# Optimization experiments

Measured on AMD Instinct MI355X. Metric: run time of the kernel, lower is better.

The kernel has to match this reference:

```python
import jax, jax.numpy as jnp
import numpy as np

N = 2048
DT = 0.016
GRAVITY = jnp.array([0.0, -9.8, 0.0], dtype=jnp.float32)


def setup_inputs() -> dict:
    key = jax.random.key(0)
    ks = jax.random.split(key, 10)

    def init_w(k, shape):
        # torch Linear default: U(-1/sqrt(fan_in), 1/sqrt(fan_in)); approximate scale
        bound = 1.0 / np.sqrt(shape[0])
        return jax.random.uniform(k, shape, jnp.float32, -bound, bound)

    return {
        "external_forces": jax.random.normal(ks[0], (N, 3), jnp.float32),
        "positions": jax.random.normal(ks[1], (N, 3), jnp.float32) * 0.1,
        "velocities": jnp.zeros((N, 3), jnp.float32),
        "mass": jnp.ones((N,), jnp.float32),
        "elasticity": jnp.full((N,), 0.8, jnp.float32),
        "friction": jnp.full((N,), 0.1, jnp.float32),
        "W1": init_w(ks[2], (8, 64)),  "b1": jnp.zeros((64,), jnp.float32),
        "W2": init_w(ks[3], (64, 64)), "b2": jnp.zeros((64,), jnp.float32),
        "W3": init_w(ks[4], (64, 32)), "b3": jnp.zeros((32,), jnp.float32),
        "W4": init_w(ks[5], (32, 3)),  "b4": jnp.zeros((3,), jnp.float32),
    }


def _force_mlp(f, W1, b1, W2, b2, W3, b3, W4, b4):
    h = jax.nn.relu(f @ W1 + b1)
    h = jax.nn.relu(h @ W2 + b2)
    h = jax.nn.relu(h @ W3 + b3)
    return jnp.tanh(h @ W4 + b4) * 10.0


def _neural_forces(positions, velocities, mass, W1, b1, W2, b2, W3, b3, W4, b4):
    # edge (i, j): features = [pos_j - pos_i, vel_j - vel_i, dist_ij, mass_i / mass_j]
    rel_pos = positions[None, :, :] - positions[:, None, :]          # [N, N, 3]
    rel_vel = velocities[None, :, :] - velocities[:, None, :]        # [N, N, 3]
    dist = jnp.linalg.norm(rel_pos, axis=-1)                          # [N, N]
    ratio = mass[:, None] / mass[None, :]                             # [N, N]
    feat = jnp.concatenate(
        [rel_pos, rel_vel, dist[..., None], ratio[..., None]], axis=-1)  # [N, N, 8]
    edge_f = _force_mlp(feat, W1, b1, W2, b2, W3, b3, W4, b4)         # [N, N, 3]
    mask = (dist < 1.0) & ~jnp.eye(dist.shape[0], dtype=bool)         # radius graph, no self-edge
    return jnp.sum(edge_f * mask[..., None], axis=1)                  # scatter-add over j -> [N, 3]


def reference(external_forces, positions, velocities, mass, elasticity, friction,
              W1, b1, W2, b2, W3, b3, W4, b4):
    forces = GRAVITY[None, :] * mass[:, None] + external_forces
    forces = forces + _neural_forces(positions, velocities, mass,
                                     W1, b1, W2, b2, W3, b3, W4, b4)
    accel = forces / mass[:, None]
    new_vel = velocities + accel * DT
    # friction applied where |v| > 0.1
    fric_mask = jnp.linalg.norm(new_vel, axis=1) > 0.1
    new_vel = new_vel + jnp.where(fric_mask[:, None],
                                  -new_vel * friction[:, None] * DT, 0.0)
    new_pos = positions + new_vel * DT
    # ground collision: clamp y, reflect vy scaled by elasticity
    coll = new_pos[:, 1] < 0.0
    new_pos = new_pos.at[:, 1].set(jnp.where(coll, 0.0, new_pos[:, 1]))
    new_vel = new_vel.at[:, 1].set(
        jnp.where(coll, -new_vel[:, 1] * elasticity, new_vel[:, 1]))
    return new_pos, new_vel
```

## Files before the change

kernel.cpp:

```cpp
#include <hip/hip_runtime.h>
#include <math.h>

#define NPART 2048
#define DT 0.016f

typedef __attribute__((ext_vector_type(8)))  short bf16x8;
typedef __attribute__((ext_vector_type(16))) float f32x16;

#define MFMA(A, B, C) __builtin_amdgcn_mfma_f32_32x32x16_bf16((A), (B), (C), 0, 0, 0)

__device__ inline unsigned cvt_pk(float lo, float hi) {
    unsigned r;
    asm("v_cvt_pk_bf16_f32 %0, %1, %2" : "=v"(r) : "v"(lo), "v"(hi));
    return r;
}
__device__ inline void swap32(unsigned &x, unsigned &y) {
    asm("v_permlane32_swap_b32 %0, %1" : "+v"(x), "+v"(y));
}
__device__ inline bf16x8 mk8(unsigned a, unsigned b, unsigned c, unsigned d) {
    union { unsigned u[4]; bf16x8 s; } u;
    u.u[0] = a; u.u[1] = b; u.u[2] = c; u.u[3] = d;
    return u.s;
}
__device__ inline bf16x8 pack8(const float f[8]) {
    return mk8(cvt_pk(f[0], f[1]), cvt_pk(f[2], f[3]), cvt_pk(f[4], f[5]), cvt_pk(f[6], f[7]));
}

__device__ inline void d2b(const f32x16 &d, bf16x8 &blo, bf16x8 &bhi) {
    float r[16];
#pragma unroll
    for (int t = 0; t < 16; ++t) r[t] = fmaxf(d[t], 0.f);
    unsigned p01 = cvt_pk(r[0], r[1]),  p23 = cvt_pk(r[2], r[3]);
    unsigned p45 = cvt_pk(r[4], r[5]),  p67 = cvt_pk(r[6], r[7]);
    swap32(p01, p45);
    swap32(p23, p67);
    blo = mk8(p01, p23, p45, p67);
    unsigned q01 = cvt_pk(r[8], r[9]),   q23 = cvt_pk(r[10], r[11]);
    unsigned q45 = cvt_pk(r[12], r[13]), q67 = cvt_pk(r[14], r[15]);
    swap32(q01, q45);
    swap32(q23, q67);
    bhi = mk8(q01, q23, q45, q67);
}

__global__ __launch_bounds__(256) void particle_step_kernel(
    const float* __restrict__ ext,  const float* __restrict__ pos,
    const float* __restrict__ vel,  const float* __restrict__ mass,
    const float* __restrict__ elast, const float* __restrict__ fric,
    const float* __restrict__ W1, const float* __restrict__ b1,
    const float* __restrict__ W2, const float* __restrict__ b2,
    const float* __restrict__ W3, const float* __restrict__ b3,
    const float* __restrict__ W4, const float* __restrict__ b4,
    float* __restrict__ out)
{
    const int l = threadIdx.x & 63;
    const int c = l & 31;
    const int h = l >> 5;
    const int w = threadIdx.x >> 6;
    const int i = blockIdx.x;

    bf16x8 a1[2];
    bf16x8 a2[2][5];
    bf16x8 a3[5];
    bf16x8 a4[3];
#pragma unroll
    for (int mt = 0; mt < 2; ++mt) {
        const int m = c + 32 * mt;
        float f[8];
        if (h == 0) {
#pragma unroll
            for (int e = 0; e < 8; ++e) f[e] = W1[e * 64 + m];
        } else {
            f[0] = b1[m];
#pragma unroll
            for (int e = 1; e < 8; ++e) f[e] = 0.f;
        }
        a1[mt] = pack8(f);
    }
#pragma unroll
    for (int mt = 0; mt < 2; ++mt) {
        const int m = c + 32 * mt;
#pragma unroll
        for (int kg = 0; kg < 4; ++kg) {
            float f[8];
#pragma unroll
            for (int e = 0; e < 8; ++e) f[e] = W2[(kg * 16 + 8 * h + e) * 64 + m];
            a2[mt][kg] = pack8(f);
        }
        float f[8];
        f[0] = (h == 0) ? b2[m] : 0.f;
#pragma unroll
        for (int e = 1; e < 8; ++e) f[e] = 0.f;
        a2[mt][4] = pack8(f);
    }
#pragma unroll
    for (int kg = 0; kg < 4; ++kg) {
        float f[8];
#pragma unroll
        for (int e = 0; e < 8; ++e) f[e] = W3[(kg * 16 + 8 * h + e) * 32 + c];
        a3[kg] = pack8(f);
    }
    {
        float f[8];
        f[0] = (h == 0) ? b3[c] : 0.f;
#pragma unroll
        for (int e = 1; e < 8; ++e) f[e] = 0.f;
        a3[4] = pack8(f);
    }
#pragma unroll
    for (int kg = 0; kg < 2; ++kg) {
        float f[8];
#pragma unroll
        for (int e = 0; e < 8; ++e) f[e] = (c < 3) ? W4[(kg * 16 + 8 * h + e) * 3 + c] : 0.f;
        a4[kg] = pack8(f);
    }
    {
        float f[8];
        f[0] = (h == 0 && c < 3) ? b4[c] : 0.f;
#pragma unroll
        for (int e = 1; e < 8; ++e) f[e] = 0.f;
        a4[2] = pack8(f);
    }

    const bf16x8 bgate = mk8((l < 32) ? 0x00003f80u : 0u, 0u, 0u, 0u);
    const f32x16 z = {};

    const float pix = pos[3 * i], piy = pos[3 * i + 1], piz = pos[3 * i + 2];
    const float vix = vel[3 * i], viy = vel[3 * i + 1], viz = vel[3 * i + 2];
    const float mi = mass[i];

    float Fx = 0.f, Fy = 0.f, Fz = 0.f;

    for (int t = 0; t < 16; ++t) {
        const int T = w * 16 + t;
        const int j = T * 32 + c;

        const float pjx = pos[3 * j], pjy = pos[3 * j + 1], pjz = pos[3 * j + 2];
        const float vjx = vel[3 * j], vjy = vel[3 * j + 1], vjz = vel[3 * j + 2];
        const float mj = mass[j];
        const float rx = pjx - pix, ry = pjy - piy, rz = pjz - piz;
        const float sx = vjx - vix, sy = vjy - viy, sz = vjz - viz;
        const float dist = sqrtf(rx * rx + ry * ry + rz * rz);
        const float ratio = mi / mj;
        const bool valid = (dist < 1.0f) && (j != i);

        bf16x8 bf;
        if (l < 32)
            bf = mk8(cvt_pk(rx, ry), cvt_pk(rz, sx), cvt_pk(sy, sz), cvt_pk(dist, ratio));
        else
            bf = mk8(0x00003f80u, 0u, 0u, 0u);

        f32x16 acc0 = MFMA(a1[0], bf, z);
        f32x16 acc1 = MFMA(a1[1], bf, z);

        bf16x8 bn[4];
        d2b(acc0, bn[0], bn[1]);
        d2b(acc1, bn[2], bn[3]);

        acc0 = MFMA(a2[0][0], bn[0], z);
        acc0 = MFMA(a2[0][1], bn[1], acc0);
        acc0 = MFMA(a2[0][2], bn[2], acc0);
        acc0 = MFMA(a2[0][3], bn[3], acc0);
        acc0 = MFMA(a2[0][4], bgate, acc0);
        acc1 = MFMA(a2[1][0], bn[0], z);
        acc1 = MFMA(a2[1][1], bn[1], acc1);
        acc1 = MFMA(a2[1][2], bn[2], acc1);
        acc1 = MFMA(a2[1][3], bn[3], acc1);
        acc1 = MFMA(a2[1][4], bgate, acc1);

        d2b(acc0, bn[0], bn[1]);
        d2b(acc1, bn[2], bn[3]);

        f32x16 acc3 = MFMA(a3[0], bn[0], z);
        acc3 = MFMA(a3[1], bn[1], acc3);
        acc3 = MFMA(a3[2], bn[2], acc3);
        acc3 = MFMA(a3[3], bn[3], acc3);
        acc3 = MFMA(a3[4], bgate, acc3);

        bf16x8 b4lo, b4hi;
        d2b(acc3, b4lo, b4hi);

        f32x16 o = MFMA(a4[0], b4lo, z);
        o = MFMA(a4[1], b4hi, o);
        o = MFMA(a4[2], bgate, o);

        if (l < 32 && valid) {
            Fx += tanhf(o[0]) * 10.f;
            Fy += tanhf(o[1]) * 10.f;
            Fz += tanhf(o[2]) * 10.f;
        }
    }

#pragma unroll
    for (int off = 1; off < 64; off <<= 1) {
        Fx += __shfl_xor(Fx, off);
        Fy += __shfl_xor(Fy, off);
        Fz += __shfl_xor(Fz, off);
    }
    __shared__ float red[4][3];
    if ((threadIdx.x & 63) == 0) { red[w][0] = Fx; red[w][1] = Fy; red[w][2] = Fz; }
    __syncthreads();

    if (threadIdx.x == 0) {
        float FX = red[0][0] + red[1][0] + red[2][0] + red[3][0];
        float FY = red[0][1] + red[1][1] + red[2][1] + red[3][1];
        float FZ = red[0][2] + red[1][2] + red[2][2] + red[3][2];

        FX += ext[3 * i + 0];
        FY += ext[3 * i + 1] + (-9.8f) * mi;
        FZ += ext[3 * i + 2];

        const float inv_m = 1.0f / mi;
        float nvx = vix + FX * inv_m * DT;
        float nvy = viy + FY * inv_m * DT;
        float nvz = viz + FZ * inv_m * DT;

        const float speed = sqrtf(nvx * nvx + nvy * nvy + nvz * nvz);
        if (speed > 0.1f) {
            const float s = fric[i] * DT;
            nvx -= nvx * s;
            nvy -= nvy * s;
            nvz -= nvz * s;
        }

        float npx = pix + nvx * DT;
        float npy = piy + nvy * DT;
        float npz = piz + nvz * DT;

        if (npy < 0.0f) {
            npy = 0.0f;
            nvy = -nvy * elast[i];
        }

        out[3 * i + 0] = npx;
        out[3 * i + 1] = npy;
        out[3 * i + 2] = npz;
        out[NPART * 3 + 3 * i + 0] = nvx;
        out[NPART * 3 + 3 * i + 1] = nvy;
        out[NPART * 3 + 3 * i + 2] = nvz;
    }
}

extern "C" void kernel_launch(void* const* d_in, const int* in_sizes, int n_in,
                              void* d_out, int out_size, void* d_ws, size_t ws_size,
                              hipStream_t stream) {
    const float* ext   = (const float*)d_in[0];
    const float* pos   = (const float*)d_in[1];
    const float* vel   = (const float*)d_in[2];
    const float* mass  = (const float*)d_in[3];
    const float* elast = (const float*)d_in[4];
    const float* fric  = (const float*)d_in[5];
    const float* W1 = (const float*)d_in[6];
    const float* b1 = (const float*)d_in[7];
    const float* W2 = (const float*)d_in[8];
    const float* b2 = (const float*)d_in[9];
    const float* W3 = (const float*)d_in[10];
    const float* b3 = (const float*)d_in[11];
    const float* W4 = (const float*)d_in[12];
    const float* b4 = (const float*)d_in[13];
    float* out = (float*)d_out;

    particle_step_kernel<<<NPART, 256, 0, stream>>>(
        ext, pos, vel, mass, elast, fric,
        W1, b1, W2, b2, W3, b3, W4, b4, out);
}
```

Baseline: 115.8 us.

## Switch MLP to fp16 MFMA and add split-precision fixup pass for boundary particles

Replaces the bf16 MFMAs with fp16 MFMAs and uses a fast exp/rcp tanh, a branchless masked accumulate, and interleaved layer-2 accumulator chains. The main kernel records the pre-clamp y position in workspace. A second kernel recomputes particles whose y lies within a small margin of zero using hi/lo split fp16 (roughly 3x MFMA work), so the ground-collision branch decision matches the fp32 reference. This adds a second launch and heavier recompute for near-boundary particles in exchange for a cheaper, more accurate main path.

```diff
diff --git a/kernel.cpp b/kernel.cpp
--- a/kernel.cpp
+++ b/kernel.cpp
@@ -3,43 +3,78 @@
 
 #define NPART 2048
 #define DT 0.016f
-
-typedef __attribute__((ext_vector_type(8)))  short bf16x8;
+#define MARGIN_EPS 2e-3f
+
+typedef _Float16 f16x8 __attribute__((ext_vector_type(8)));
 typedef __attribute__((ext_vector_type(16))) float f32x16;
 
-#define MFMA(A, B, C) __builtin_amdgcn_mfma_f32_32x32x16_bf16((A), (B), (C), 0, 0, 0)
-
-__device__ inline unsigned cvt_pk(float lo, float hi) {
-    unsigned r;
-    asm("v_cvt_pk_bf16_f32 %0, %1, %2" : "=v"(r) : "v"(lo), "v"(hi));
-    return r;
+#define MFMA(A, B, C) __builtin_amdgcn_mfma_f32_32x32x16_f16((A), (B), (C), 0, 0, 0)
+
+__device__ inline unsigned pk16(float lo, float hi) {
+    union { _Float16 h[2]; unsigned u; } x;
+    x.h[0] = (_Float16)lo; x.h[1] = (_Float16)hi;
+    return x.u;
 }
 __device__ inline void swap32(unsigned &x, unsigned &y) {
     asm("v_permlane32_swap_b32 %0, %1" : "+v"(x), "+v"(y));
 }
-__device__ inline bf16x8 mk8(unsigned a, unsigned b, unsigned c, unsigned d) {
-    union { unsigned u[4]; bf16x8 s; } u;
+__device__ inline f16x8 mk8(unsigned a, unsigned b, unsigned c, unsigned d) {
+    union { unsigned u[4]; f16x8 s; } u;
     u.u[0] = a; u.u[1] = b; u.u[2] = c; u.u[3] = d;
     return u.s;
 }
-__device__ inline bf16x8 pack8(const float f[8]) {
-    return mk8(cvt_pk(f[0], f[1]), cvt_pk(f[2], f[3]), cvt_pk(f[4], f[5]), cvt_pk(f[6], f[7]));
-}
-
-__device__ inline void d2b(const f32x16 &d, bf16x8 &blo, bf16x8 &bhi) {
+__device__ inline f16x8 pack8(const float f[8]) {
+    return mk8(pk16(f[0], f[1]), pk16(f[2], f[3]), pk16(f[4], f[5]), pk16(f[6], f[7]));
+}
+
+__device__ inline float tanh10(float x) {
+    float e;
+    asm("v_exp_f32 %0, %1" : "=v"(e) : "v"(x * 2.885390081777927f));
+    float r;
+    asm("v_rcp_f32 %0, %1" : "=v"(r) : "v"(e + 1.0f));
+    return fmaf(-20.f, r, 10.f);
+}
+
+__device__ inline void d2b(const f32x16 &d, f16x8 &blo, f16x8 &bhi) {
     float r[16];
 #pragma unroll
     for (int t = 0; t < 16; ++t) r[t] = fmaxf(d[t], 0.f);
-    unsigned p01 = cvt_pk(r[0], r[1]),  p23 = cvt_pk(r[2], r[3]);
-    unsigned p45 = cvt_pk(r[4], r[5]),  p67 = cvt_pk(r[6], r[7]);
+    unsigned p01 = pk16(r[0], r[1]),  p23 = pk16(r[2], r[3]);
+    unsigned p45 = pk16(r[4], r[5]),  p67 = pk16(r[6], r[7]);
     swap32(p01, p45);
     swap32(p23, p67);
     blo = mk8(p01, p23, p45, p67);
-    unsigned q01 = cvt_pk(r[8], r[9]),   q23 = cvt_pk(r[10], r[11]);
-    unsigned q45 = cvt_pk(r[12], r[13]), q67 = cvt_pk(r[14], r[15]);
+    unsigned q01 = pk16(r[8], r[9]),   q23 = pk16(r[10], r[11]);
+    unsigned q45 = pk16(r[12], r[13]), q67 = pk16(r[14], r[15]);
     swap32(q01, q45);
     swap32(q23, q67);
     bhi = mk8(q01, q23, q45, q67);
+}
+
+__device__ inline void d2b_split(const f32x16 &d, f16x8 &h0, f16x8 &h1, f16x8 &l0, f16x8 &l1) {
+    float r[16];
+#pragma unroll
+    for (int t = 0; t < 16; ++t) r[t] = fmaxf(d[t], 0.f);
+    unsigned ph[8], pl[8];
+#pragma unroll
+    for (int q = 0; q < 8; ++q) {
+        const float a = r[2 * q], b = r[2 * q + 1];
+        const _Float16 ha = (_Float16)a, hb = (_Float16)b;
+        union { _Float16 h[2]; unsigned u; } up;
+        up.h[0] = ha; up.h[1] = hb;
+        ph[q] = up.u;
+        union { _Float16 h[2]; unsigned u; } ul;
+        ul.h[0] = (_Float16)(a - (float)ha); ul.h[1] = (_Float16)(b - (float)hb);
+        pl[q] = ul.u;
+    }
+    swap32(ph[0], ph[2]); swap32(ph[1], ph[3]);
+    h0 = mk8(ph[0], ph[1], ph[2], ph[3]);
+    swap32(ph[4], ph[6]); swap32(ph[5], ph[7]);
+    h1 = mk8(ph[4], ph[5], ph[6], ph[7]);
+    swap32(pl[0], pl[2]); swap32(pl[1], pl[3]);
+    l0 = mk8(pl[0], pl[1], pl[2], pl[3]);
+    swap32(pl[4], pl[6]); swap32(pl[5], pl[7]);
+    l1 = mk8(pl[4], pl[5], pl[6], pl[7]);
 }
 
 __global__ __launch_bounds__(256) void particle_step_kernel(
@@ -50,7 +85,7 @@
     const float* __restrict__ W2, const float* __restrict__ b2,
     const float* __restrict__ W3, const float* __restrict__ b3,
     const float* __restrict__ W4, const float* __restrict__ b4,
-    float* __restrict__ out)
+    float* __restrict__ out, float* __restrict__ ws)
 {
     const int l = threadIdx.x & 63;
     const int c = l & 31;
@@ -58,10 +93,7 @@
     const int w = threadIdx.x >> 6;
     const int i = blockIdx.x;
 
-    bf16x8 a1[2];
-    bf16x8 a2[2][5];
-    bf16x8 a3[5];
-    bf16x8 a4[3];
+    f16x8 a1[2], a2[2][5], a3[5], a4[3];
 #pragma unroll
     for (int mt = 0; mt < 2; ++mt) {
         const int m = c + 32 * mt;
@@ -121,7 +153,7 @@
         a4[2] = pack8(f);
     }
 
-    const bf16x8 bgate = mk8((l < 32) ? 0x00003f80u : 0u, 0u, 0u, 0u);
+    const f16x8 bgate = mk8((l < 32) ? 0x00003C00u : 0u, 0u, 0u, 0u);
     const f32x16 z = {};
 
     const float pix = pos[3 * i], piy = pos[3 * i + 1], piz = pos[3 * i + 2];
@@ -131,40 +163,41 @@
     float Fx = 0.f, Fy = 0.f, Fz = 0.f;
 
     for (int t = 0; t < 16; ++t) {
-        const int T = w * 16 + t;
-        const int j = T * 32 + c;
+        const int j = (w * 16 + t) * 32 + c;
 
         const float pjx = pos[3 * j], pjy = pos[3 * j + 1], pjz = pos[3 * j + 2];
         const float vjx = vel[3 * j], vjy = vel[3 * j + 1], vjz = vel[3 * j + 2];
         const float mj = mass[j];
         const float rx = pjx - pix, ry = pjy - piy, rz = pjz - piz;
         const float sx = vjx - vix, sy = vjy - viy, sz = vjz - viz;
-        const float dist = sqrtf(rx * rx + ry * ry + rz * rz);
-        const float ratio = mi / mj;
-        const bool valid = (dist < 1.0f) && (j != i);
-
-        bf16x8 bf;
-        if (l < 32)
-            bf = mk8(cvt_pk(rx, ry), cvt_pk(rz, sx), cvt_pk(sy, sz), cvt_pk(dist, ratio));
-        else
-            bf = mk8(0x00003f80u, 0u, 0u, 0u);
+        const float d2 = rx * rx + ry * ry + rz * rz;
+        const float dist = __builtin_amdgcn_sqrtf(d2);
+        const float ratio = mi * __builtin_amdgcn_rcpf(mj);
+        const float sel = (l < 32 && dist < 1.0f && j != i) ? 1.0f : 0.0f;
+
+        const unsigned d0 = pk16(rx, ry), d1 = pk16(rz, sx);
+        const unsigned d2p = pk16(sy, sz), d3 = pk16(dist, ratio);
+        const f16x8 bf = mk8((l < 32) ? d0 : 0x00003C00u,
+                             (l < 32) ? d1 : 0u,
+                             (l < 32) ? d2p : 0u,
+                             (l < 32) ? d3 : 0u);
 
         f32x16 acc0 = MFMA(a1[0], bf, z);
         f32x16 acc1 = MFMA(a1[1], bf, z);
 
-        bf16x8 bn[4];
+        f16x8 bn[4];
         d2b(acc0, bn[0], bn[1]);
         d2b(acc1, bn[2], bn[3]);
 
         acc0 = MFMA(a2[0][0], bn[0], z);
+        acc1 = MFMA(a2[1][0], bn[0], z);
         acc0 = MFMA(a2[0][1], bn[1], acc0);
+        acc1 = MFMA(a2[1][1], bn[1], acc1);
         acc0 = MFMA(a2[0][2], bn[2], acc0);
+        acc1 = MFMA(a2[1][2], bn[2], acc1);
         acc0 = MFMA(a2[0][3], bn[3], acc0);
+        acc1 = MFMA(a2[1][3], bn[3], acc1);
         acc0 = MFMA(a2[0][4], bgate, acc0);
-        acc1 = MFMA(a2[1][0], bn[0], z);
-        acc1 = MFMA(a2[1][1], bn[1], acc1);
-        acc1 = MFMA(a2[1][2], bn[2], acc1);
-        acc1 = MFMA(a2[1][3], bn[3], acc1);
         acc1 = MFMA(a2[1][4], bgate, acc1);
 
         d2b(acc0, bn[0], bn[1]);
@@ -176,18 +209,244 @@
         acc3 = MFMA(a3[3], bn[3], acc3);
         acc3 = MFMA(a3[4], bgate, acc3);
 
-        bf16x8 b4lo, b4hi;
+        f16x8 b4lo, b4hi;
         d2b(acc3, b4lo, b4hi);
 
         f32x16 o = MFMA(a4[0], b4lo, z);
         o = MFMA(a4[1], b4hi, o);
         o = MFMA(a4[2], bgate, o);
 
-        if (l < 32 && valid) {
-            Fx += tanhf(o[0]) * 10.f;
-            Fy += tanhf(o[1]) * 10.f;
-            Fz += tanhf(o[2]) * 10.f;
-        }
+        Fx = fmaf(sel, tanh10(o[0]), Fx);
+        Fy = fmaf(sel, tanh10(o[1]), Fy);
+        Fz = fmaf(sel, tanh10(o[2]), Fz);
+    }
+
+#pragma unroll
+    for (int off = 1; off < 64; off <<= 1) {
+        Fx += __shfl_xor(Fx, off);
+        Fy += __shfl_xor(Fy, off);
+        Fz += __shfl_xor(Fz, off);
+    }
+    __shared__ float red[4][3];
+    if ((threadIdx.x & 63) == 0) { red[w][0] = Fx; red[w][1] = Fy; red[w][2] = Fz; }
+    __syncthreads();
+
+    if (threadIdx.x == 0) {
+        float FX = red[0][0] + red[1][0] + red[2][0] + red[3][0];
+        float FY = red[0][1] + red[1][1] + red[2][1] + red[3][1];
+        float FZ = red[0][2] + red[1][2] + red[2][2] + red[3][2];
+
+        FX += ext[3 * i + 0];
+        FY += ext[3 * i + 1] + (-9.8f) * mi;
+        FZ += ext[3 * i + 2];
+
+        const float inv_m = 1.0f / mi;
+        float nvx = vix + FX * inv_m * DT;
+        float nvy = viy + FY * inv_m * DT;
+        float nvz = viz + FZ * inv_m * DT;
+
+        const float speed = sqrtf(nvx * nvx + nvy * nvy + nvz * nvz);
+        if (speed > 0.1f) {
+            const float s = fric[i] * DT;
+            nvx -= nvx * s;
+            nvy -= nvy * s;
+            nvz -= nvz * s;
+        }
+
+        float npx = pix + nvx * DT;
+        float npy = piy + nvy * DT;
+        float npz = piz + nvz * DT;
+
+        ws[i] = npy;
+
+        if (npy < 0.0f) {
+            npy = 0.0f;
+            nvy = -nvy * elast[i];
+        }
+
+        out[3 * i + 0] = npx;
+        out[3 * i + 1] = npy;
+        out[3 * i + 2] = npz;
+        out[NPART * 3 + 3 * i + 0] = nvx;
+        out[NPART * 3 + 3 * i + 1] = nvy;
+        out[NPART * 3 + 3 * i + 2] = nvz;
+    }
+}
+
+__global__ __launch_bounds__(256, 1) void particle_fix_kernel(
+    const float* __restrict__ ext,  const float* __restrict__ pos,
+    const float* __restrict__ vel,  const float* __restrict__ mass,
+    const float* __restrict__ elast, const float* __restrict__ fric,
+    const float* __restrict__ W1, const float* __restrict__ b1,
+    const float* __restrict__ W2, const float* __restrict__ b2,
+    const float* __restrict__ W3, const float* __restrict__ b3,
+    const float* __restrict__ W4, const float* __restrict__ b4,
+    float* __restrict__ out, const float* __restrict__ ws)
+{
+    const int i = blockIdx.x;
+    if (fabsf(ws[i]) >= MARGIN_EPS) return;
+
+    const int l = threadIdx.x & 63;
+    const int c = l & 31;
+    const int h = l >> 5;
+    const int w = threadIdx.x >> 6;
+
+    f16x8 a1h[2], a1l[2];
+    f16x8 a2h[2][4], a2l[2][4];
+    f16x8 a3h[4], a3l[4];
+    f16x8 a4h[2], a4l[2];
+#pragma unroll
+    for (int mt = 0; mt < 2; ++mt) {
+        const int m = c + 32 * mt;
+        float fh[8], fl[8];
+#pragma unroll
+        for (int e = 0; e < 8; ++e) {
+            const float v = W1[e * 64 + m];
+            const float vh = (float)(_Float16)v;
+            fh[e] = vh; fl[e] = v - vh;
+        }
+        a1h[mt] = pack8(fh); a1l[mt] = pack8(fl);
+    }
+#pragma unroll
+    for (int mt = 0; mt < 2; ++mt) {
+        const int m = c + 32 * mt;
+#pragma unroll
+        for (int kg = 0; kg < 4; ++kg) {
+            float fh[8], fl[8];
+#pragma unroll
+            for (int e = 0; e < 8; ++e) {
+                const float v = W2[(kg * 16 + 8 * h + e) * 64 + m];
+                const float vh = (float)(_Float16)v;
+                fh[e] = vh; fl[e] = v - vh;
+            }
+            a2h[mt][kg] = pack8(fh); a2l[mt][kg] = pack8(fl);
+        }
+    }
+#pragma unroll
+    for (int kg = 0; kg < 4; ++kg) {
+        float fh[8], fl[8];
+#pragma unroll
+        for (int e = 0; e < 8; ++e) {
+            const float v = W3[(kg * 16 + 8 * h + e) * 32 + c];
+            const float vh = (float)(_Float16)v;
+            fh[e] = vh; fl[e] = v - vh;
+        }
+        a3h[kg] = pack8(fh); a3l[kg] = pack8(fl);
+    }
+#pragma unroll
+    for (int kg = 0; kg < 2; ++kg) {
+        float fh[8], fl[8];
+#pragma unroll
+        for (int e = 0; e < 8; ++e) {
+            const float v = (c < 3) ? W4[(kg * 16 + 8 * h + e) * 3 + c] : 0.f;
+            const float vh = (float)(_Float16)v;
+            fh[e] = vh; fl[e] = v - vh;
+        }
+        a4h[kg] = pack8(fh); a4l[kg] = pack8(fl);
+    }
+
+    f32x16 cb1a, cb1b, cb2a, cb2b, cb3, cb4;
+#pragma unroll
+    for (int t = 0; t < 16; ++t) {
+        const int row = (t & 3) + 8 * (t >> 2) + 4 * h;
+        cb1a[t] = b1[row];       cb1b[t] = b1[32 + row];
+        cb2a[t] = b2[row];       cb2b[t] = b2[32 + row];
+        cb3[t]  = b3[row];
+        cb4[t]  = (row < 3) ? b4[row] : 0.f;
+    }
+
+    const float pix = pos[3 * i], piy = pos[3 * i + 1], piz = pos[3 * i + 2];
+    const float vix = vel[3 * i], viy = vel[3 * i + 1], viz = vel[3 * i + 2];
+    const float mi = mass[i];
+
+    float Fx = 0.f, Fy = 0.f, Fz = 0.f;
+
+    for (int t = 0; t < 16; ++t) {
+        const int j = (w * 16 + t) * 32 + c;
+
+        const float pjx = pos[3 * j], pjy = pos[3 * j + 1], pjz = pos[3 * j + 2];
+        const float vjx = vel[3 * j], vjy = vel[3 * j + 1], vjz = vel[3 * j + 2];
+        const float mj = mass[j];
+        const float rx = pjx - pix, ry = pjy - piy, rz = pjz - piz;
+        const float sx = vjx - vix, sy = vjy - viy, sz = vjz - viz;
+        const float d2 = rx * rx + ry * ry + rz * rz;
+        const float dist = sqrtf(d2);
+        const float ratio = mi / mj;
+        const float sel = (l < 32 && dist < 1.0f && j != i) ? 1.0f : 0.0f;
+
+        float f8[8] = { rx, ry, rz, sx, sy, sz, dist, ratio };
+        float fh[8], fl[8];
+#pragma unroll
+        for (int e = 0; e < 8; ++e) {
+            const float vh = (float)(_Float16)f8[e];
+            fh[e] = vh; fl[e] = f8[e] - vh;
+        }
+        const f16x8 bfh = pack8(fh), bfl = pack8(fl);
+        const f16x8 bf = (l < 32) ? bfh : bfl;
+
+        f32x16 acc0 = MFMA(a1h[0], bf, cb1a);
+        acc0 = MFMA(a1l[0], bf, acc0);
+        f32x16 acc1 = MFMA(a1h[1], bf, cb1b);
+        acc1 = MFMA(a1l[1], bf, acc1);
+
+        f16x8 bh0, bh1, bh2, bh3, bl0, bl1, bl2, bl3;
+        d2b_split(acc0, bh0, bh1, bl0, bl1);
+        d2b_split(acc1, bh2, bh3, bl2, bl3);
+
+        acc0 = MFMA(a2h[0][0], bh0, cb2a);
+        acc0 = MFMA(a2h[0][1], bh1, acc0);
+        acc0 = MFMA(a2h[0][2], bh2, acc0);
+        acc0 = MFMA(a2h[0][3], bh3, acc0);
+        acc0 = MFMA(a2h[0][0], bl0, acc0);
+        acc0 = MFMA(a2h[0][1], bl1, acc0);
+        acc0 = MFMA(a2h[0][2], bl2, acc0);
+        acc0 = MFMA(a2h[0][3], bl3, acc0);
+        acc0 = MFMA(a2l[0][0], bh0, acc0);
+        acc0 = MFMA(a2l[0][1], bh1, acc0);
+        acc0 = MFMA(a2l[0][2], bh2, acc0);
+        acc0 = MFMA(a2l[0][3], bh3, acc0);
+        acc1 = MFMA(a2h[1][0], bh0, cb2b);
+        acc1 = MFMA(a2h[1][1], bh1, acc1);
+        acc1 = MFMA(a2h[1][2], bh2, acc1);
+        acc1 = MFMA(a2h[1][3], bh3, acc1);
+        acc1 = MFMA(a2h[1][0], bl0, acc1);
+        acc1 = MFMA(a2h[1][1], bl1, acc1);
+        acc1 = MFMA(a2h[1][2], bl2, acc1);
+        acc1 = MFMA(a2h[1][3], bl3, acc1);
+        acc1 = MFMA(a2l[1][0], bh0, acc1);
+        acc1 = MFMA(a2l[1][1], bh1, acc1);
+        acc1 = MFMA(a2l[1][2], bh2, acc1);
+        acc1 = MFMA(a2l[1][3], bh3, acc1);
+
+        d2b_split(acc0, bh0, bh1, bl0, bl1);
+        d2b_split(acc1, bh2, bh3, bl2, bl3);
+
+        f32x16 acc3 = MFMA(a3h[0], bh0, cb3);
+        acc3 = MFMA(a3h[1], bh1, acc3);
+        acc3 = MFMA(a3h[2], bh2, acc3);
+        acc3 = MFMA(a3h[3], bh3, acc3);
+        acc3 = MFMA(a3h[0], bl0, acc3);
+        acc3 = MFMA(a3h[1], bl1, acc3);
+        acc3 = MFMA(a3h[2], bl2, acc3);
+        acc3 = MFMA(a3h[3], bl3, acc3);
+        acc3 = MFMA(a3l[0], bh0, acc3);
+        acc3 = MFMA(a3l[1], bh1, acc3);
+        acc3 = MFMA(a3l[2], bh2, acc3);
+        acc3 = MFMA(a3l[3], bh3, acc3);
+
+        f16x8 th0, th1, tl0, tl1;
+        d2b_split(acc3, th0, th1, tl0, tl1);
+
+        f32x16 o = MFMA(a4h[0], th0, cb4);
+        o = MFMA(a4h[1], th1, o);
+        o = MFMA(a4h[0], tl0, o);
+        o = MFMA(a4h[1], tl1, o);
+        o = MFMA(a4l[0], th0, o);
+        o = MFMA(a4l[1], th1, o);
+
+        Fx = fmaf(sel, tanhf(o[0]) * 10.f, Fx);
+        Fy = fmaf(sel, tanhf(o[1]) * 10.f, Fy);
+        Fz = fmaf(sel, tanhf(o[2]) * 10.f, Fz);
     }
 
 #pragma unroll
@@ -258,8 +517,12 @@
     const float* W4 = (const float*)d_in[12];
     const float* b4 = (const float*)d_in[13];
     float* out = (float*)d_out;
+    float* wsf = (float*)d_ws;
 
     particle_step_kernel<<<NPART, 256, 0, stream>>>(
         ext, pos, vel, mass, elast, fric,
-        W1, b1, W2, b2, W3, b3, W4, b4, out);
-}
+        W1, b1, W2, b2, W3, b3, W4, b4, out, wsf);
+    particle_fix_kernel<<<NPART, 256, 0, stream>>>(
+        ext, pos, vel, mass, elast, fric,
+        W1, b1, W2, b2, W3, b3, W4, b4, out, wsf);
+}
```

Measured after the change: 177.3 us. 1.53x slower.
